# Performance work log

Measured on AMD Instinct MI355X. Metric: run time of the kernel, lower is better.

Reference implementation:

```python
import jax, jax.numpy as jnp
import numpy as np

NEG = -1e30  # log(0) surrogate that stays finite in fp32
BLANK = 0


def setup_inputs() -> dict:
    key = jax.random.key(0)
    k1, k2 = jax.random.split(key)
    B, T, V, L = 32, 1024, 1024, 256
    logits = jax.random.normal(k1, (B, T, V), dtype=jnp.float32)
    log_probs = jax.nn.log_softmax(logits, axis=-1)  # module expects log-probs
    labels = jax.random.randint(k2, (B, L), 1, V, dtype=jnp.int32)  # avoid blank=0
    input_lens = jnp.full((B,), T, dtype=jnp.int32)
    label_lens = jnp.full((B,), L, dtype=jnp.int32)
    return {"log_probs": log_probs, "labels": labels,
            "input_lens": input_lens, "label_lens": label_lens}


def _ctc_loss_sum(log_probs, labels, input_lens, label_lens, blank=BLANK):
    """CTC forward DP (alpha recursion) in log space; reduction='sum', zero_infinity=True."""
    B, T, V = log_probs.shape
    L = labels.shape[1]
    S = 2 * L + 1  # extended label: blank l1 blank l2 ... blank

    ext = jnp.full((B, S), blank, dtype=labels.dtype)
    ext = ext.at[:, 1::2].set(labels)
    # skip transition s-2 -> s allowed iff ext[s] != blank and ext[s] != ext[s-2]
    skip = jnp.concatenate(
        [jnp.zeros((B, 2), dtype=bool),
         (ext[:, 2:] != blank) & (ext[:, 2:] != ext[:, :-2])], axis=1)

    lp_tbv = jnp.transpose(log_probs, (1, 0, 2))  # 'btv->tbv' as in the module

    emit0 = jnp.take_along_axis(lp_tbv[0], ext, axis=1)  # [B,S]
    alpha0 = jnp.full((B, S), NEG, dtype=log_probs.dtype)
    alpha0 = alpha0.at[:, 0].set(emit0[:, 0]).at[:, 1].set(emit0[:, 1])

    neg1 = jnp.full((B, 1), NEG, dtype=log_probs.dtype)
    neg2 = jnp.full((B, 2), NEG, dtype=log_probs.dtype)

    def step(alpha, inputs):
        lp_t, t = inputs  # lp_t: [B,V]
        em = jnp.take_along_axis(lp_t, ext, axis=1)  # [B,S]
        a1 = alpha
        a2 = jnp.concatenate([neg1, alpha[:, :-1]], axis=1)
        a3 = jnp.where(skip, jnp.concatenate([neg2, alpha[:, :-2]], axis=1), NEG)
        new = jnp.logaddexp(jnp.logaddexp(a1, a2), a3) + em
        # freeze alpha once past this sample's input length
        new = jnp.where((t < input_lens)[:, None], new, alpha)
        return new, None

    ts = jnp.arange(1, T)
    alpha, _ = jax.lax.scan(step, alpha0, (lp_tbv[1:], ts))

    s_last = 2 * label_lens  # final blank state index per sample
    a_last = jnp.take_along_axis(alpha, s_last[:, None], axis=1)[:, 0]
    a_prev = jnp.take_along_axis(alpha, (s_last - 1)[:, None], axis=1)[:, 0]
    loss_b = -jnp.logaddexp(a_last, a_prev)
    loss_b = jnp.where(loss_b > 1e29, 0.0, loss_b)  # zero_infinity=True
    return jnp.sum(loss_b)


def reference(log_probs, labels, input_lens, label_lens):
    return _ctc_loss_sum(log_probs, labels, input_lens, label_lens)
```

## Files before the change

### kernel.cpp

```cpp
#include <hip/hip_runtime.h>


constexpr int B_ = 32, T_ = 1024, V_ = 1024, L_ = 256;
constexpr int S_ = 2 * L_ + 1;
constexpr int CH = 16;
constexpr int NCHUNK = 64;
constexpr float LN2F = 0.6931471805599453f;

typedef const __attribute__((address_space(1))) unsigned int* gp_t;
typedef __attribute__((address_space(3))) unsigned int* lp_t;

__global__ __launch_bounds__(256, 4) void ctc_gather(
    float* __restrict__ lp, const int* __restrict__ labels,
    float* __restrict__ blanks)
{
    const int wave = threadIdx.x >> 6;
    const int lane = threadIdx.x & 63;
    const int r = blockIdx.x * 4 + wave;
    const int b = r >> 10;
    float* row = lp + (size_t)r * V_;
    const int* labb = labels + b * L_;

    const int4 e = *(const int4*)(labb + 4 * lane);
    const float v0 = row[e.x];
    const float v1 = row[e.y];
    const float v2 = row[e.z];
    const float v3 = row[e.w];
    const float vb = row[0];
    float4 q;
    q.x = __expf(v0); q.y = __expf(v1); q.z = __expf(v2); q.w = __expf(v3);
    const float qb = __expf(vb);
    __syncthreads();
    *(float4*)(row + 4 * lane) = q;
    if (lane == 0) blanks[r] = qb;
}

__global__ __launch_bounds__(64, 1) void ctc_dp(
    const float* __restrict__ Q, const float* __restrict__ blanks,
    const int* __restrict__ labels, const int* __restrict__ input_lens,
    const int* __restrict__ label_lens, float* __restrict__ out)
{
    __shared__ float blk[T_];
    __shared__ float buf[2][CH][256];
    __shared__ float Ls[S_];
    const int b    = blockIdx.x;
    const int lane = threadIdx.x;
    const float* Qb  = Q + (size_t)b * T_ * V_;
    const float* blg = blanks + b * T_;
    const int*  labb = labels + b * L_;
    const int il = input_lens[b];
    const int ll = label_lens[b];
    const int tend = il < T_ ? il : T_;

    #pragma unroll
    for (int i = 0; i < 4; ++i)
        __builtin_amdgcn_global_load_lds((gp_t)(blg + 256 * i + 4 * lane),
                                         (lp_t)&blk[256 * i], 16, 0, 0);
    #pragma unroll
    for (int i = 0; i < CH; ++i) {
        int t = 1 + i; if (t > T_ - 1) t = T_ - 1;
        __builtin_amdgcn_global_load_lds((gp_t)(Qb + (size_t)t * V_ + 4 * lane),
                                         (lp_t)&buf[0][i][0], 16, 0, 0);
    }

    const int4 e  = *(const int4*)(labb + 4 * lane);
    const int  ep = (lane > 0) ? labb[4 * lane - 1] : -1;
    const float kf0 = ((8 * lane + 1) >= 3 && e.x != ep) ? 1.f : 0.f;
    const float kf1 = (e.y != e.x) ? 1.f : 0.f;
    const float kf2 = (e.z != e.y) ? 1.f : 0.f;
    const float kf3 = (e.w != e.z) ? 1.f : 0.f;

    float p0 = 0.f, p1 = 0.f, p2 = 0.f, p3 = 0.f, p4 = 0.f,
          p5 = 0.f, p6 = 0.f, p7 = 0.f, p8 = 0.f;
    if (lane == 0) { p0 = blg[0]; p1 = Qb[0]; }
    int Esc = 0;
    float pm1 = 0.f;

    auto rescale = [&]() {
        float m = fmaxf(fmaxf(fmaxf(fmaxf(p0, p1), fmaxf(p2, p3)),
                              fmaxf(fmaxf(p4, p5), fmaxf(p6, p7))), p8);
        #pragma unroll
        for (int off = 32; off >= 1; off >>= 1)
            m = fmaxf(m, __shfl_xor(m, off));
        const unsigned eb = (__float_as_uint(m) >> 23) & 0xffu;
        if (eb >= 1u && eb <= 253u) {
            const float sf = __uint_as_float((254u - eb) << 23);
            p0 *= sf; p1 *= sf; p2 *= sf; p3 *= sf; p4 *= sf;
            p5 *= sf; p6 *= sf; p7 *= sf; p8 *= sf; pm1 *= sf;
            Esc += 127 - (int)eb;
        }
    };

    for (int c = 0; c < NCHUNK; ++c) {
        const int cb = c & 1;
        if (c + 1 < NCHUNK) {
            #pragma unroll
            for (int i = 0; i < CH; ++i) {
                int t = 1 + (c + 1) * CH + i; if (t > T_ - 1) t = T_ - 1;
                __builtin_amdgcn_global_load_lds(
                    (gp_t)(Qb + (size_t)t * V_ + 4 * lane),
                    (lp_t)&buf[cb ^ 1][i][0], 16, 0, 0);
            }
            asm volatile("s_waitcnt vmcnt(16)" ::: "memory");
        } else {
            asm volatile("s_waitcnt vmcnt(0)" ::: "memory");
        }
        #pragma unroll
        for (int i = 0; i < CH; ++i) {
            const int t = 1 + c * CH + i;
            if (t < tend) {
                const float4 q  = *(const float4*)&buf[cb][i][4 * lane];
                const float  qb = blk[t];
                const float n0 = (p0 + pm1) * qb;
                const float n1 = fmaf(kf0, pm1, p1 + p0) * q.x;
                const float n2 = (p2 + p1) * qb;
                const float n3 = fmaf(kf1, p1, p3 + p2) * q.y;
                const float n4 = (p4 + p3) * qb;
                const float n5 = fmaf(kf2, p3, p5 + p4) * q.z;
                const float n6 = (p6 + p5) * qb;
                const float n7 = fmaf(kf3, p5, p7 + p6) * q.w;
                const float n8 = (p8 + p7) * qb;
                p0 = n0; p1 = n1; p2 = n2; p3 = n3; p4 = n4;
                p5 = n5; p6 = n6; p7 = n7; p8 = n8;
                pm1 = __shfl_up(p7, 1);
                if (lane == 0) pm1 = 0.f;
            }
            if (i == 7) rescale();
        }
        rescale();
    }

    Ls[8 * lane + 0] = p0; Ls[8 * lane + 1] = p1;
    Ls[8 * lane + 2] = p2; Ls[8 * lane + 3] = p3;
    Ls[8 * lane + 4] = p4; Ls[8 * lane + 5] = p5;
    Ls[8 * lane + 6] = p6; Ls[8 * lane + 7] = p7;
    if (lane == 63) Ls[512] = p8;
    __syncthreads();
    if (lane == 0) {
        const int sl = 2 * ll;
        const float la  = Ls[sl];
        const float lb  = (sl >= 1) ? Ls[sl - 1] : 0.f;
        const float tot = la + lb;
        float loss = (float)Esc * LN2F - __logf(tot);
        if (!(loss <= 1e29f)) loss = 0.f;
        atomicAdd(out, loss);
    }
}

extern "C" void kernel_launch(void* const* d_in, const int* in_sizes, int n_in,
                              void* d_out, int out_size, void* d_ws, size_t ws_size,
                              hipStream_t stream) {
    float*       lp     = (float*)d_in[0];
    const int*   labels = (const int*)d_in[1];
    const int*   il     = (const int*)d_in[2];
    const int*   ll     = (const int*)d_in[3];
    float* out    = (float*)d_out;
    float* blanks = (float*)d_ws;

    hipMemsetAsync(out, 0, sizeof(float), stream);
    ctc_gather<<<dim3(B_ * T_ / 4), dim3(256), 0, stream>>>(lp, labels, blanks);
    ctc_dp<<<dim3(B_), dim3(64), 0, stream>>>(lp, blanks, labels, il, ll, out);
}
```

Baseline: 365.3 us.

## Replace LDS-staged prefetch with register triple-buffered global loads in CTC DP

```diff
diff --git a/kernel.cpp b/kernel.cpp
--- a/kernel.cpp
+++ b/kernel.cpp
@@ -3,8 +3,6 @@
 
 constexpr int B_ = 32, T_ = 1024, V_ = 1024, L_ = 256;
 constexpr int S_ = 2 * L_ + 1;
-constexpr int CH = 16;
-constexpr int NCHUNK = 64;
 constexpr float LN2F = 0.6931471805599453f;
 
 typedef const __attribute__((address_space(1))) unsigned int* gp_t;
@@ -41,7 +39,6 @@
     const int* __restrict__ label_lens, float* __restrict__ out)
 {
     __shared__ float blk[T_];
-    __shared__ float buf[2][CH][256];
     __shared__ float Ls[S_];
     const int b    = blockIdx.x;
     const int lane = threadIdx.x;
@@ -56,12 +53,6 @@
     for (int i = 0; i < 4; ++i)
         __builtin_amdgcn_global_load_lds((gp_t)(blg + 256 * i + 4 * lane),
                                          (lp_t)&blk[256 * i], 16, 0, 0);
-    #pragma unroll
-    for (int i = 0; i < CH; ++i) {
-        int t = 1 + i; if (t > T_ - 1) t = T_ - 1;
-        __builtin_amdgcn_global_load_lds((gp_t)(Qb + (size_t)t * V_ + 4 * lane),
-                                         (lp_t)&buf[0][i][0], 16, 0, 0);
-    }
 
     const int4 e  = *(const int4*)(labb + 4 * lane);
     const int  ep = (lane > 0) ? labb[4 * lane - 1] : -1;
@@ -75,6 +66,20 @@
     if (lane == 0) { p0 = blg[0]; p1 = Qb[0]; }
     int Esc = 0;
     float pm1 = 0.f;
+
+    float4 bufA[8], bufB[8], bufC[8];
+
+#define ISSUE(c, BUF)                                                        \
+    do {                                                                     \
+        __builtin_amdgcn_sched_barrier(0);                                   \
+        _Pragma("unroll")                                                    \
+        for (int ii = 0; ii < 8; ++ii) {                                     \
+            int tt = 1 + (c) * 8 + ii;                                       \
+            if (tt > T_ - 1) tt = T_ - 1;                                    \
+            BUF[ii] = *(const float4*)(Qb + (size_t)tt * V_ + 4 * lane);     \
+        }                                                                    \
+        __builtin_amdgcn_sched_barrier(0);                                   \
+    } while (0)
 
     auto rescale = [&]() {
         float m = fmaxf(fmaxf(fmaxf(fmaxf(p0, p1), fmaxf(p2, p3)),
@@ -91,44 +96,44 @@
         }
     };
 
-    for (int c = 0; c < NCHUNK; ++c) {
-        const int cb = c & 1;
-        if (c + 1 < NCHUNK) {
-            #pragma unroll
-            for (int i = 0; i < CH; ++i) {
-                int t = 1 + (c + 1) * CH + i; if (t > T_ - 1) t = T_ - 1;
-                __builtin_amdgcn_global_load_lds(
-                    (gp_t)(Qb + (size_t)t * V_ + 4 * lane),
-                    (lp_t)&buf[cb ^ 1][i][0], 16, 0, 0);
-            }
-            asm volatile("s_waitcnt vmcnt(16)" ::: "memory");
-        } else {
-            asm volatile("s_waitcnt vmcnt(0)" ::: "memory");
-        }
-        #pragma unroll
-        for (int i = 0; i < CH; ++i) {
-            const int t = 1 + c * CH + i;
-            if (t < tend) {
-                const float4 q  = *(const float4*)&buf[cb][i][4 * lane];
-                const float  qb = blk[t];
-                const float n0 = (p0 + pm1) * qb;
-                const float n1 = fmaf(kf0, pm1, p1 + p0) * q.x;
-                const float n2 = (p2 + p1) * qb;
-                const float n3 = fmaf(kf1, p1, p3 + p2) * q.y;
-                const float n4 = (p4 + p3) * qb;
-                const float n5 = fmaf(kf2, p3, p5 + p4) * q.z;
-                const float n6 = (p6 + p5) * qb;
-                const float n7 = fmaf(kf3, p5, p7 + p6) * q.w;
-                const float n8 = (p8 + p7) * qb;
-                p0 = n0; p1 = n1; p2 = n2; p3 = n3; p4 = n4;
-                p5 = n5; p6 = n6; p7 = n7; p8 = n8;
-                pm1 = __shfl_up(p7, 1);
-                if (lane == 0) pm1 = 0.f;
-            }
-            if (i == 7) rescale();
-        }
-        rescale();
+#define COMPUTE(c, BUF)                                                      \
+    do {                                                                     \
+        _Pragma("unroll")                                                    \
+        for (int ii = 0; ii < 8; ++ii) {                                     \
+            const int t = 1 + (c) * 8 + ii;                                  \
+            if (t < tend) {                  \
+                const float4 q  = BUF[ii];                                   \
+                const float  qb = blk[t];             \
+                const float n0 = (p0 + pm1) * qb;                            \
+                const float n1 = fmaf(kf0, pm1, p1 + p0) * q.x;              \
+                const float n2 = (p2 + p1) * qb;                             \
+                const float n3 = fmaf(kf1, p1, p3 + p2) * q.y;               \
+                const float n4 = (p4 + p3) * qb;                             \
+                const float n5 = fmaf(kf2, p3, p5 + p4) * q.z;               \
+                const float n6 = (p6 + p5) * qb;                             \
+                const float n7 = fmaf(kf3, p5, p7 + p6) * q.w;               \
+                const float n8 = (p8 + p7) * qb;    \
+                p0 = n0; p1 = n1; p2 = n2; p3 = n3; p4 = n4;                 \
+                p5 = n5; p6 = n6; p7 = n7; p8 = n8;                          \
+                pm1 = __shfl_up(p7, 1);                                      \
+                if (lane == 0) pm1 = 0.f;                                    \
+            }                                                                \
+        }                                                                    \
+        rescale();                                                           \
+    } while (0)
+
+    ISSUE(0, bufA);
+    ISSUE(1, bufB);
+    for (int c = 0; c < 129; c += 3) {
+        ISSUE(c + 2, bufC);
+        COMPUTE(c, bufA);
+        ISSUE(c + 3, bufA);
+        COMPUTE(c + 1, bufB);
+        ISSUE(c + 4, bufB);
+        COMPUTE(c + 2, bufC);
     }
+#undef ISSUE
+#undef COMPUTE
 
     Ls[8 * lane + 0] = p0; Ls[8 * lane + 1] = p1;
     Ls[8 * lane + 2] = p2; Ls[8 * lane + 3] = p3;
```

Measured after the change: 340.8 us. -6.7%, faster.

## Split CTC DP into producer/consumer waves with 4-deep LDS ring buffer

Applied to the files above, without the earlier changes.

```diff
diff --git a/kernel.cpp b/kernel.cpp
--- a/kernel.cpp
+++ b/kernel.cpp
@@ -5,6 +5,7 @@
 constexpr int S_ = 2 * L_ + 1;
 constexpr int CH = 16;
 constexpr int NCHUNK = 64;
+constexpr int NBUF = 4;
 constexpr float LN2F = 0.6931471805599453f;
 
 typedef const __attribute__((address_space(1))) unsigned int* gp_t;
@@ -32,19 +33,24 @@
     const float qb = __expf(vb);
     __syncthreads();
     *(float4*)(row + 4 * lane) = q;
-    if (lane == 0) blanks[r] = qb;
+    if (lane == 0) {
+        const int t = r & (T_ - 1);
+        blanks[(r & ~(T_ - 1)) + ((t + T_ - 1) & (T_ - 1))] = qb;
+    }
 }
 
-__global__ __launch_bounds__(64, 1) void ctc_dp(
+__global__ __launch_bounds__(128) void ctc_dp(
     const float* __restrict__ Q, const float* __restrict__ blanks,
     const int* __restrict__ labels, const int* __restrict__ input_lens,
     const int* __restrict__ label_lens, float* __restrict__ out)
 {
     __shared__ float blk[T_];
-    __shared__ float buf[2][CH][256];
-    __shared__ float Ls[S_];
+    __shared__ float buf[NBUF][CH][256];
+    __shared__ int Pf, Cf;
     const int b    = blockIdx.x;
-    const int lane = threadIdx.x;
+    const int tid  = threadIdx.x;
+    const int lane = tid & 63;
+    const int wv   = tid >> 6;
     const float* Qb  = Q + (size_t)b * T_ * V_;
     const float* blg = blanks + b * T_;
     const int*  labb = labels + b * L_;
@@ -52,98 +58,126 @@
     const int ll = label_lens[b];
     const int tend = il < T_ ? il : T_;
 
-    #pragma unroll
-    for (int i = 0; i < 4; ++i)
-        __builtin_amdgcn_global_load_lds((gp_t)(blg + 256 * i + 4 * lane),
-                                         (lp_t)&blk[256 * i], 16, 0, 0);
-    #pragma unroll
-    for (int i = 0; i < CH; ++i) {
-        int t = 1 + i; if (t > T_ - 1) t = T_ - 1;
-        __builtin_amdgcn_global_load_lds((gp_t)(Qb + (size_t)t * V_ + 4 * lane),
-                                         (lp_t)&buf[0][i][0], 16, 0, 0);
-    }
+    if (tid == 0) { Pf = 0; Cf = 0; }
+    __syncthreads();
 
-    const int4 e  = *(const int4*)(labb + 4 * lane);
-    const int  ep = (lane > 0) ? labb[4 * lane - 1] : -1;
-    const float kf0 = ((8 * lane + 1) >= 3 && e.x != ep) ? 1.f : 0.f;
-    const float kf1 = (e.y != e.x) ? 1.f : 0.f;
-    const float kf2 = (e.z != e.y) ? 1.f : 0.f;
-    const float kf3 = (e.w != e.z) ? 1.f : 0.f;
+    if (wv == 1) {
+        #pragma unroll
+        for (int i = 0; i < 4; ++i)
+            __builtin_amdgcn_global_load_lds((gp_t)(blg + 256 * i + 4 * lane),
+                                             (lp_t)&blk[256 * i], 16, 0, 0);
+        #pragma unroll
+        for (int i = 0; i < CH; ++i) {
+            int t = 1 + i; if (t > T_ - 1) t = T_ - 1;
+            __builtin_amdgcn_global_load_lds(
+                (gp_t)(Qb + (size_t)t * V_ + 4 * lane),
+                (lp_t)&buf[0][i][0], 16, 0, 0);
+        }
+        for (int c = 0; c < NCHUNK; ++c) {
+            if (c + 1 < NCHUNK) {
+                while (__hip_atomic_load(&Cf, __ATOMIC_ACQUIRE,
+                                         __HIP_MEMORY_SCOPE_WORKGROUP) < c + 2 - NBUF) {}
+                const int cb = (c + 1) & (NBUF - 1);
+                #pragma unroll
+                for (int i = 0; i < CH; ++i) {
+                    int t = 1 + (c + 1) * CH + i; if (t > T_ - 1) t = T_ - 1;
+                    __builtin_amdgcn_global_load_lds(
+                        (gp_t)(Qb + (size_t)t * V_ + 4 * lane),
+                        (lp_t)&buf[cb][i][0], 16, 0, 0);
+                }
+                asm volatile("s_waitcnt vmcnt(16)" ::: "memory");
+            } else {
+                asm volatile("s_waitcnt vmcnt(0)" ::: "memory");
+            }
+            if (lane == 0)
+                __hip_atomic_store(&Pf, c + 1, __ATOMIC_RELEASE,
+                                   __HIP_MEMORY_SCOPE_WORKGROUP);
+        }
+    } else {
+        const int4 e  = *(const int4*)(labb + 4 * lane);
+        const int  ep = (lane > 0) ? labb[4 * lane - 1] : -1;
+        const float kf0 = ((8 * lane + 1) >= 3 && e.x != ep) ? 1.f : 0.f;
+        const float kf1 = (e.y != e.x) ? 1.f : 0.f;
+        const float kf2 = (e.z != e.y) ? 1.f : 0.f;
+        const float kf3 = (e.w != e.z) ? 1.f : 0.f;
+        const float bl0 = blg[T_ - 1];
+        const float q00 = Qb[0];
+        float p0 = (lane == 0) ? bl0 : 0.f;
+        float p1 = (lane == 0) ? q00 : 0.f;
+        float p2 = 0.f, p3 = 0.f, p4 = 0.f, p5 = 0.f,
+              p6 = 0.f, p7 = 0.f, p8 = 0.f;
+        int Esc = 0;
+        float pm1 = 0.f;
 
-    float p0 = 0.f, p1 = 0.f, p2 = 0.f, p3 = 0.f, p4 = 0.f,
-          p5 = 0.f, p6 = 0.f, p7 = 0.f, p8 = 0.f;
-    if (lane == 0) { p0 = blg[0]; p1 = Qb[0]; }
-    int Esc = 0;
-    float pm1 = 0.f;
+        auto rescale = [&]() {
+            float m = fmaxf(fmaxf(fmaxf(fmaxf(p0, p1), fmaxf(p2, p3)),
+                                  fmaxf(fmaxf(p4, p5), fmaxf(p6, p7))), p8);
+            #pragma unroll
+            for (int off = 32; off >= 1; off >>= 1)
+                m = fmaxf(m, __shfl_xor(m, off));
+            const unsigned eb = (__float_as_uint(m) >> 23) & 0xffu;
+            if (eb >= 1u && eb <= 253u) {
+                const float sf = __uint_as_float((254u - eb) << 23);
+                p0 *= sf; p1 *= sf; p2 *= sf; p3 *= sf; p4 *= sf;
+                p5 *= sf; p6 *= sf; p7 *= sf; p8 *= sf; pm1 *= sf;
+                Esc += 127 - (int)eb;
+            }
+        };
 
-    auto rescale = [&]() {
-        float m = fmaxf(fmaxf(fmaxf(fmaxf(p0, p1), fmaxf(p2, p3)),
-                              fmaxf(fmaxf(p4, p5), fmaxf(p6, p7))), p8);
-        #pragma unroll
-        for (int off = 32; off >= 1; off >>= 1)
-            m = fmaxf(m, __shfl_xor(m, off));
-        const unsigned eb = (__float_as_uint(m) >> 23) & 0xffu;
-        if (eb >= 1u && eb <= 253u) {
-            const float sf = __uint_as_float((254u - eb) << 23);
-            p0 *= sf; p1 *= sf; p2 *= sf; p3 *= sf; p4 *= sf;
-            p5 *= sf; p6 *= sf; p7 *= sf; p8 *= sf; pm1 *= sf;
-            Esc += 127 - (int)eb;
-        }
-    };
-
-    for (int c = 0; c < NCHUNK; ++c) {
-        const int cb = c & 1;
-        if (c + 1 < NCHUNK) {
+        for (int c = 0; c < NCHUNK; ++c) {
+            while (__hip_atomic_load(&Pf, __ATOMIC_ACQUIRE,
+                                     __HIP_MEMORY_SCOPE_WORKGROUP) <= c) {}
+            const float* bufc = &buf[c & (NBUF - 1)][0][0];
+            float4 bv;
             #pragma unroll
             for (int i = 0; i < CH; ++i) {
-                int t = 1 + (c + 1) * CH + i; if (t > T_ - 1) t = T_ - 1;
-                __builtin_amdgcn_global_load_lds(
-                    (gp_t)(Qb + (size_t)t * V_ + 4 * lane),
-                    (lp_t)&buf[cb ^ 1][i][0], 16, 0, 0);
+                if ((i & 3) == 0) bv = *(const float4*)&blk[c * CH + i];
+                const float qb = ((i & 3) == 0) ? bv.x : ((i & 3) == 1) ? bv.y
+                               : ((i & 3) == 2) ? bv.z : bv.w;
+                const int t = 1 + c * CH + i;
+                if (t < tend) {
+                    const float4 q = *(const float4*)(bufc + i * 256 + 4 * lane);
+                    const float n0 = (p0 + pm1) * qb;
+                    const float n1 = fmaf(kf0, pm1, p1 + p0) * q.x;
+                    const float n2 = (p2 + p1) * qb;
+                    const float n3 = fmaf(kf1, p1, p3 + p2) * q.y;
+                    const float n4 = (p4 + p3) * qb;
+                    const float n5 = fmaf(kf2, p3, p5 + p4) * q.z;
+                    const float n6 = (p6 + p5) * qb;
+                    const float n7 = fmaf(kf3, p5, p7 + p6) * q.w;
+                    const float n8 = (p8 + p7) * qb;
+                    p0 = n0; p1 = n1; p2 = n2; p3 = n3; p4 = n4;
+                    p5 = n5; p6 = n6; p7 = n7; p8 = n8;
+                    pm1 = __shfl_up(p7, 1);
+                    if (lane == 0) pm1 = 0.f;
+                }
+                if (i == 7) rescale();
             }
-            asm volatile("s_waitcnt vmcnt(16)" ::: "memory");
-        } else {
-            asm volatile("s_waitcnt vmcnt(0)" ::: "memory");
+            rescale();
+            if (lane == 0)
+                __hip_atomic_store(&Cf, c + 1, __ATOMIC_RELEASE,
+                                   __HIP_MEMORY_SCOPE_WORKGROUP);
         }
-        #pragma unroll
-        for (int i = 0; i < CH; ++i) {
-            const int t = 1 + c * CH + i;
-            if (t < tend) {
-                const float4 q  = *(const float4*)&buf[cb][i][4 * lane];
-                const float  qb = blk[t];
-                const float n0 = (p0 + pm1) * qb;
-                const float n1 = fmaf(kf0, pm1, p1 + p0) * q.x;
-                const float n2 = (p2 + p1) * qb;
-                const float n3 = fmaf(kf1, p1, p3 + p2) * q.y;
-                const float n4 = (p4 + p3) * qb;
-                const float n5 = fmaf(kf2, p3, p5 + p4) * q.z;
-                const float n6 = (p6 + p5) * qb;
-                const float n7 = fmaf(kf3, p5, p7 + p6) * q.w;
-                const float n8 = (p8 + p7) * qb;
-                p0 = n0; p1 = n1; p2 = n2; p3 = n3; p4 = n4;
-                p5 = n5; p6 = n6; p7 = n7; p8 = n8;
-                pm1 = __shfl_up(p7, 1);
-                if (lane == 0) pm1 = 0.f;
-            }
-            if (i == 7) rescale();
+
+        const int sl = 2 * ll;
+        auto pick = [&](int s) -> float {
+            if (s == 512) return __shfl(p8, 63);
+            const int r = s & 7;
+            float v = p0;
+            v = (r == 1) ? p1 : v; v = (r == 2) ? p2 : v;
+            v = (r == 3) ? p3 : v; v = (r == 4) ? p4 : v;
+            v = (r == 5) ? p5 : v; v = (r == 6) ? p6 : v;
+            v = (r == 7) ? p7 : v;
+            return __shfl(v, s >> 3);
+        };
+        const float la = pick(sl);
+        const float lb = pick(sl - 1);
+        if (lane == 0) {
+            const float tot = la + lb;
+            float loss = (float)Esc * LN2F - __logf(tot);
+            if (!(loss <= 1e29f)) loss = 0.f;
+            atomicAdd(out, loss);
         }
-        rescale();
-    }
-
-    Ls[8 * lane + 0] = p0; Ls[8 * lane + 1] = p1;
-    Ls[8 * lane + 2] = p2; Ls[8 * lane + 3] = p3;
-    Ls[8 * lane + 4] = p4; Ls[8 * lane + 5] = p5;
-    Ls[8 * lane + 6] = p6; Ls[8 * lane + 7] = p7;
-    if (lane == 63) Ls[512] = p8;
-    __syncthreads();
-    if (lane == 0) {
-        const int sl = 2 * ll;
-        const float la  = Ls[sl];
-        const float lb  = (sl >= 1) ? Ls[sl - 1] : 0.f;
-        const float tot = la + lb;
-        float loss = (float)Esc * LN2F - __logf(tot);
-        if (!(loss <= 1e29f)) loss = 0.f;
-        atomicAdd(out, loss);
     }
 }
 
@@ -159,5 +193,5 @@
 
     hipMemsetAsync(out, 0, sizeof(float), stream);
     ctc_gather<<<dim3(B_ * T_ / 4), dim3(256), 0, stream>>>(lp, labels, blanks);
-    ctc_dp<<<dim3(B_), dim3(64), 0, stream>>>(lp, blanks, labels, il, ll, out);
+    ctc_dp<<<dim3(B_), dim3(128), 0, stream>>>(lp, blanks, labels, il, ll, out);
 }
```

Result: faster. 342.5 us (-6.2%).
